# Performance work log

Measured on AMD Instinct MI355X. Metric: run time of the kernel, lower is better.

## Reference

```python
import jax, jax.numpy as jnp
import numpy as np

Q, B, D, NH, DH, DI, M = 1024, 4, 1024, 16, 64, 4096, 1024
K = Q + M  # klen
SCALE_W = 0.02
LN_EPS = 1e-5


def _layer_norm(x, g, b):
    mu = jnp.mean(x, axis=-1, keepdims=True)
    var = jnp.var(x, axis=-1, keepdims=True)
    return (x - mu) * jax.lax.rsqrt(var + LN_EPS) * g + b


def _rel_shift(x):
    # x: [qlen, klen, bsz, n_head] -> Transformer-XL relative shift
    q, k = x.shape[0], x.shape[1]
    zero_pad = jnp.zeros((q, 1) + x.shape[2:], x.dtype)
    x_padded = jnp.concatenate([zero_pad, x], axis=1)          # [q, k+1, b, n]
    x_padded = x_padded.reshape((k + 1, q) + x.shape[2:])      # [k+1, q, b, n]
    return x_padded[1:].reshape(x.shape)


def setup_inputs() -> dict:
    key = jax.random.key(0)
    ks = jax.random.split(key, 12)
    f32 = jnp.float32
    inp = {
        "w": jax.random.normal(ks[0], (Q, B, D), f32),
        "r": jax.random.normal(ks[1], (K, 1, D), f32),
        "mems": jax.random.normal(ks[2], (M, B, D), f32),
        "qkv_w": SCALE_W * jax.random.normal(ks[3], (D, 3 * NH * DH), f32),
        "r_net_w": SCALE_W * jax.random.normal(ks[4], (D, NH * DH), f32),
        "o_w": SCALE_W * jax.random.normal(ks[5], (NH * DH, D), f32),
        "r_w_bias": SCALE_W * jax.random.normal(ks[6], (NH, DH), f32),
        "r_r_bias": SCALE_W * jax.random.normal(ks[7], (NH, DH), f32),
        "ln1_g": jnp.ones((D,), f32),
        "ln1_b": jnp.zeros((D,), f32),
        "ff_w1": SCALE_W * jax.random.normal(ks[8], (D, DI), f32),
        "ff_b1": jnp.zeros((DI,), f32),
        "ff_w2": SCALE_W * jax.random.normal(ks[9], (DI, D), f32),
        "ff_b2": jnp.zeros((D,), f32),
        "ln2_g": jnp.ones((D,), f32),
        "ln2_b": jnp.zeros((D,), f32),
        # causal mask with memory: query i attends to keys j <= i + mem_len
        "attn_mask": jnp.arange(K)[None, :] > (jnp.arange(Q)[:, None] + M),
    }
    return inp


def reference(w, r, mems, qkv_w, r_net_w, o_w, r_w_bias, r_r_bias,
              ln1_g, ln1_b, ff_w1, ff_b1, ff_w2, ff_b2, ln2_g, ln2_b,
              attn_mask):
    qlen, bsz = w.shape[0], w.shape[1]
    # --- relative multi-head attention (post-lnorm, mems concat) ---
    cat = jnp.concatenate([mems, w], axis=0)                   # [klen, b, d]
    w_heads = cat @ qkv_w                                      # [klen, b, 3*nh*dh]
    r_head_k = (r @ r_net_w).reshape(-1, NH, DH)               # [rlen, nh, dh]
    q_h, k_h, v_h = jnp.split(w_heads, 3, axis=-1)
    klen = k_h.shape[0]
    q_h = q_h[-qlen:].reshape(qlen, bsz, NH, DH)
    k_h = k_h.reshape(klen, bsz, NH, DH)
    v_h = v_h.reshape(klen, bsz, NH, DH)

    rw_q = q_h + r_w_bias[None, None]                          # [q, b, nh, dh]
    AC = jnp.einsum('ibnd,jbnd->ijbn', rw_q, k_h)
    rr_q = q_h + r_r_bias[None, None]
    BD = jnp.einsum('ibnd,jnd->ijbn', rr_q, r_head_k)
    BD = _rel_shift(BD)

    scale = 1.0 / (DH ** 0.5)
    attn_score = (AC + BD) * scale                             # [q, k, b, nh]
    attn_score = jnp.where(attn_mask[:, :, None, None], -jnp.inf, attn_score)
    attn_prob = jax.nn.softmax(attn_score, axis=1)
    attn_vec = jnp.einsum('ijbn,jbnd->ibnd', attn_prob, v_h)
    attn_out = attn_vec.reshape(qlen, bsz, NH * DH) @ o_w      # [q, b, d]
    out = _layer_norm(w + attn_out, ln1_g, ln1_b)

    # --- position-wise FFN (post-lnorm) ---
    core = jax.nn.relu(out @ ff_w1 + ff_b1) @ ff_w2 + ff_b2
    out = _layer_norm(out + core, ln2_g, ln2_b)
    return out
```

## Files before the change

kernel.cpp:

```cpp
#include <hip/hip_runtime.h>
#include <math.h>


#define QLEN 1024
#define BSZ  4
#define DMODEL 1024
#define NHEAD 16
#define DHEAD 64
#define DINNER 4096
#define MEMLEN 1024
#define KLEN 2048

typedef __attribute__((ext_vector_type(8))) short short8;
typedef __attribute__((ext_vector_type(4))) short short4_t;
typedef __attribute__((ext_vector_type(4))) float f32x4;

__device__ __forceinline__ unsigned short f2bf(float x) {
  union { float f; unsigned u; } cv; cv.f = x;
  const unsigned u = cv.u;
  return (unsigned short)((u + 0x7FFFu + ((u >> 16) & 1u)) >> 16);
}
__device__ __forceinline__ float bf2f(unsigned short b) {
  union { unsigned u; float f; } cv; cv.u = ((unsigned)b) << 16;
  return cv.f;
}

__device__ __forceinline__ void gload16(const void* g, void* l) {
  __builtin_amdgcn_global_load_lds(
      (const __attribute__((address_space(1))) unsigned int*)g,
      (__attribute__((address_space(3))) unsigned int*)l, 16, 0, 0);
}

__device__ __forceinline__ int chidx(int row, int kc) {
  return row * 4 + (kc ^ ((row >> 1) & 3));
}

template<int MODE, int TN>
__global__ __launch_bounds__(256) void mgemm(
    const unsigned short* __restrict__ A, const unsigned short* __restrict__ Bt,
    float* __restrict__ C, unsigned short* __restrict__ Cb,
    const float* __restrict__ aux, const float* __restrict__ res,
    unsigned short* __restrict__ oK, unsigned short* __restrict__ oV,
    int Kdim, int N)
{
  __shared__ __align__(16) char smem[8192 + TN * 64];

  const int tid = threadIdx.x;
  const int lane = tid & 63, wv = tid >> 6;
  const int m0 = (int)blockIdx.y * 128, n0 = (int)blockIdx.x * TN;

  const unsigned short *gA0, *gA1, *gB0, *gB1 = nullptr;
  {
    int c = tid, m = c >> 2, kc = (c & 3) ^ ((m >> 1) & 3);
    gA0 = A + (size_t)(m0 + m) * Kdim + kc * 8;
    c = 256 + tid; m = c >> 2; kc = (c & 3) ^ ((m >> 1) & 3);
    gA1 = A + (size_t)(m0 + m) * Kdim + kc * 8;
    c = tid; int nn = c >> 2; kc = (c & 3) ^ ((nn >> 1) & 3);
    gB0 = Bt + (size_t)(n0 + nn) * Kdim + kc * 8;
    if constexpr (TN == 128) {
      c = 256 + tid; nn = c >> 2; kc = (c & 3) ^ ((nn >> 1) & 3);
      gB1 = Bt + (size_t)(n0 + nn) * Kdim + kc * 8;
    }
  }
  char* const lds0 = smem + (tid & 192) * 16;

  const int fr = lane & 15, kq = lane >> 4;
  constexpr int NJ = TN / 32;
  int aoff[4], boff[NJ];
#pragma unroll
  for (int t = 0; t < 4; ++t) {
    const int ra = (wv & 1) * 64 + t * 16 + fr;
    aoff[t] = chidx(ra, kq) * 16;
  }
#pragma unroll
  for (int t = 0; t < NJ; ++t) {
    const int rb = (wv >> 1) * (TN / 2) + t * 16 + fr;
    boff[t] = 8192 + chidx(rb, kq) * 16;
  }

  f32x4 acc[4][NJ] = {};

  for (int k0 = 0; k0 < Kdim; k0 += 32) {
    gload16(gA0, lds0);
    gload16(gA1, lds0 + 4096);
    gload16(gB0, lds0 + 8192);
    if constexpr (TN == 128) gload16(gB1, lds0 + 12288);
    gA0 += 32; gA1 += 32; gB0 += 32;
    if constexpr (TN == 128) gB1 += 32;
    __syncthreads();

    short8 af[4], bf[NJ];
#pragma unroll
    for (int t = 0; t < 4; ++t) af[t] = *(const short8*)(smem + aoff[t]);
#pragma unroll
    for (int t = 0; t < NJ; ++t) bf[t] = *(const short8*)(smem + boff[t]);
#pragma unroll
    for (int i = 0; i < 4; ++i)
#pragma unroll
      for (int j = 0; j < NJ; ++j)
        acc[i][j] = __builtin_amdgcn_mfma_f32_16x16x32_bf16(
            af[i], bf[j], acc[i][j], 0, 0, 0);
    __syncthreads();
  }

  const int rbase = m0 + (wv & 1) * 64 + (lane >> 4) * 4;
  const int cbase = n0 + (wv >> 1) * (TN / 2) + (lane & 15);
#pragma unroll
  for (int i = 0; i < 4; ++i) {
#pragma unroll
    for (int r = 0; r < 4; ++r) {
      const int grow = rbase + i * 16 + r;
#pragma unroll
      for (int j = 0; j < NJ; ++j) {
        const int gcol = cbase + j * 16;
        const float v = acc[i][j][r];
        if constexpr (MODE == 0) {
          const int kkg = grow >> 2, b2 = grow & 3;
          const int sec = gcol >> 10, hn = (gcol >> 6) & 15, d = gcol & 63;
          const unsigned short bv = f2bf(v);
          if (sec == 0) {
            if (kkg >= MEMLEN)
              Cb[((size_t)(b2 * NHEAD + hn) * QLEN + (kkg - MEMLEN)) * DHEAD + d] = bv;
          } else if (sec == 1) {
            oK[((size_t)(b2 * NHEAD + hn) * KLEN + kkg) * DHEAD + d] = bv;
          } else {
            oV[((size_t)(b2 * NHEAD + hn) * KLEN + kkg) * DHEAD + d] = bv;
          }
        } else if constexpr (MODE == 1) {
          const int hn = gcol >> 6, d = gcol & 63;
          Cb[((size_t)hn * KLEN + grow) * DHEAD + d] = f2bf(v);
        } else if constexpr (MODE == 2) {
          C[(size_t)grow * N + gcol] = v + res[(size_t)grow * N + gcol];
        } else if constexpr (MODE == 3) {
          Cb[(size_t)grow * N + gcol] = f2bf(fmaxf(v + aux[gcol], 0.f));
        } else {
          C[(size_t)grow * N + gcol] = v + aux[gcol] + res[(size_t)grow * N + gcol];
        }
      }
    }
  }
}

__global__ __launch_bounds__(256) void transpose_v(
    const unsigned short* __restrict__ Vh, unsigned short* __restrict__ Vt)
{
  __shared__ unsigned short t[64 * 80];
  const int j0 = (int)blockIdx.x * 64;
  const int bn = (int)blockIdx.y;
  const int tid = threadIdx.x;
#pragma unroll
  for (int it = 0; it < 2; ++it) {
    const int f = it * 256 + tid;
    const int j = f >> 3, d8 = (f & 7) * 8;
    const short8 v = *(const short8*)(Vh + ((size_t)bn * KLEN + j0 + j) * DHEAD + d8);
    *(short8*)(t + j * 80 + d8) = v;
  }
  __syncthreads();
  const int d = tid >> 2, jseg = (tid & 3) * 16;
  short8 o0, o1;
#pragma unroll
  for (int e = 0; e < 8; ++e) o0[e] = (short)t[(jseg + e) * 80 + d];
#pragma unroll
  for (int e = 0; e < 8; ++e) o1[e] = (short)t[(jseg + 8 + e) * 80 + d];
  unsigned short* op = Vt + ((size_t)bn * DHEAD + d) * KLEN + j0 + jseg;
  *(short8*)op = o0;
  *(short8*)(op + 8) = o1;
}

__global__ __launch_bounds__(256) void cast_all(
    const float* __restrict__ mems, const float* __restrict__ w,
    const float* __restrict__ r, unsigned short* __restrict__ Xcat,
    unsigned short* __restrict__ Rb16)
{
  const size_t i = ((size_t)blockIdx.x * 256 + threadIdx.x) * 8;
  const float* src;
  unsigned short* dst;
  if (i < 4194304)       { src = mems + i;          dst = Xcat + i; }
  else if (i < 8388608)  { src = w + (i - 4194304); dst = Xcat + i; }
  else                   { src = r + (i - 8388608); dst = Rb16 + (i - 8388608); }
  const float4 x = *(const float4*)src;
  const float4 y = *(const float4*)(src + 4);
  short8 v;
  v[0] = (short)f2bf(x.x); v[1] = (short)f2bf(x.y);
  v[2] = (short)f2bf(x.z); v[3] = (short)f2bf(x.w);
  v[4] = (short)f2bf(y.x); v[5] = (short)f2bf(y.y);
  v[6] = (short)f2bf(y.z); v[7] = (short)f2bf(y.w);
  *(short8*)dst = v;
}

__global__ __launch_bounds__(256) void transpose_all(
    const float* __restrict__ qkv_w, const float* __restrict__ r_net_w,
    const float* __restrict__ o_w, const float* __restrict__ ff_w1,
    const float* __restrict__ ff_w2,
    unsigned short* __restrict__ Wqkv, unsigned short* __restrict__ Wr,
    unsigned short* __restrict__ Wo, unsigned short* __restrict__ W1,
    unsigned short* __restrict__ W2)
{
  const int bid = (int)blockIdx.x;
  const float* in; unsigned short* out; int R, C, xt, loc;
  if (bid < 768)        { in = qkv_w;   out = Wqkv; R = 1024; C = 3072; xt = 48; loc = bid; }
  else if (bid < 1024)  { in = r_net_w; out = Wr;   R = 1024; C = 1024; xt = 16; loc = bid - 768; }
  else if (bid < 1280)  { in = o_w;     out = Wo;   R = 1024; C = 1024; xt = 16; loc = bid - 1024; }
  else if (bid < 2304)  { in = ff_w1;   out = W1;   R = 1024; C = 4096; xt = 64; loc = bid - 1280; }
  else                  { in = ff_w2;   out = W2;   R = 4096; C = 1024; xt = 16; loc = bid - 2304; }
  const int c0 = (loc % xt) * 64, r0 = (loc / xt) * 64;

  __shared__ float t[64][65];
  const int tid = threadIdx.x;
  const int rr = tid >> 4, cc = (tid & 15) * 4;
#pragma unroll
  for (int it = 0; it < 4; ++it) {
    const int rw = rr + it * 16;
    const float4 v = *(const float4*)(in + (size_t)(r0 + rw) * C + c0 + cc);
    t[rw][cc] = v.x; t[rw][cc + 1] = v.y; t[rw][cc + 2] = v.z; t[rw][cc + 3] = v.w;
  }
  __syncthreads();
  const int oc = tid >> 2, ob = (tid & 3) * 16;
#pragma unroll
  for (int j4 = 0; j4 < 4; ++j4) {
    short4_t o;
#pragma unroll
    for (int j = 0; j < 4; ++j) o[j] = (short)f2bf(t[ob + j4 * 4 + j][oc]);
    *(short4_t*)(out + (size_t)(c0 + oc) * R + r0 + ob + j4 * 4) = o;
  }
}

__global__ __launch_bounds__(256, 2) void attn_mfma(
    const unsigned short* __restrict__ Qh, const unsigned short* __restrict__ Kh,
    const unsigned short* __restrict__ Vt, const unsigned short* __restrict__ Rk,
    const float* __restrict__ rwb, const float* __restrict__ rrb,
    float* __restrict__ Opart0, float* __restrict__ Opart1,
    float* __restrict__ den0, float* __restrict__ den1)
{
  __shared__ __align__(16) char smem[65536];

  const int tid = threadIdx.x;
  const int lane = tid & 63, wv = tid >> 6;
  const int quad = lane >> 4, l15 = lane & 15;

  const int bid0 = (int)blockIdx.y * 32 + (int)blockIdx.x;
  const int slot = bid0 >> 3;
  const int bn = (bid0 & 7) * 8 + (slot >> 5);
  const int inner = slot & 31;
  const int it = inner >> 1, sp = inner & 1;
  const int i0 = it * 64;
  const int n = bn & 15;

  const int nch = 17 + it;
  const int h = (nch + 1) >> 1;
  const int lo = sp ? h : 0, hi = sp ? nch : h;

  const unsigned short* __restrict__ Qb = Qh + (size_t)bn * QLEN * DHEAD;
  const unsigned short* __restrict__ Kb = Kh + (size_t)bn * KLEN * DHEAD;
  const unsigned short* __restrict__ Vb = Vt + (size_t)bn * DHEAD * KLEN;
  const unsigned short* __restrict__ Rb = Rk + (size_t)n * KLEN * DHEAD;

  short8 qk[2], qr[2];
  {
    const int qrow = i0 + wv * 16 + l15;
    const unsigned short* qp = Qb + (size_t)qrow * DHEAD + quad * 8;
    const float* wp = rwb + n * DHEAD + quad * 8;
    const float* rp = rrb + n * DHEAD + quad * 8;
#pragma unroll
    for (int ks = 0; ks < 2; ++ks) {
      const short8 q8 = *(const short8*)(qp + ks * 32);
#pragma unroll
      for (int e = 0; e < 8; ++e) {
        const float qv = bf2f((unsigned short)q8[e]);
        qk[ks][e] = (short)f2bf(qv + wp[ks * 32 + e]);
        qr[ks][e] = (short)f2bf(qv + rp[ks * 32 + e]);
      }
    }
  }

  int srcl[4];
  bool condE[4];
#pragma unroll
  for (int r = 0; r < 4; ++r) {
    const int E = l15 - quad * 4 - r + 15;
    srcl[r] = (lane & 48) | (E & 15);
    condE[r] = (E >= 16);
  }

  f32x4 O[4] = {};
  float rden[4] = {0.f, 0.f, 0.f, 0.f};
  const int wvoff = (tid & 192) * 16;

  {
    const int j0 = lo * 64;
    const int g64 = lo - it + 15;
    const int rb3 = (g64 % 3) * 64;
#pragma unroll
    for (int t2 = 0; t2 < 2; ++t2) {
      const int s = t2 * 256 + tid;
      const int row = s >> 3, kc = (s & 7) ^ (row & 7);
      gload16(Kb + (((size_t)(j0 + row)) << 6) + kc * 8,
              smem + t2 * 4096 + wvoff);
    }
#pragma unroll
    for (int t2 = 0; t2 < 2; ++t2) {
      const int s = t2 * 256 + tid;
      const int row = s >> 3, kc = (s & 7) ^ (row & 7);
      gload16(Vb + (((size_t)row) << 11) + j0 + kc * 8,
              smem + 16384 + t2 * 4096 + wvoff);
    }
    const int gw = j0 - i0 + 960;
#pragma unroll
    for (int t2 = 0; t2 < 4; ++t2) {
      const int rr = t2 * 32 + (tid >> 3);
      const int gr = gw + rr;
      const int kc = (tid & 7) ^ (rr & 7);
      int pb = rb3 + t2 * 32; if (pb >= 192) pb -= 192;
      gload16(Rb + (((size_t)gr) << 6) + kc * 8,
              smem + 32768 + pb * 128 + wvoff);
    }
  }

  int cur = 0;
  for (int ch = lo; ch < hi; ++ch) {
    const int j0 = ch * 64;
    const int g64 = ch - it + 15;
    const int rb3 = (g64 % 3) * 64;
    const int gw = j0 - i0 + 960;

    asm volatile("s_waitcnt lgkmcnt(0)" ::: "memory");
    __builtin_amdgcn_s_barrier();

    if (ch + 1 < hi) {
      const int nb = cur ^ 1;
      const int j0n = j0 + 64;
#pragma unroll
      for (int t2 = 0; t2 < 2; ++t2) {
        const int s = t2 * 256 + tid;
        const int row = s >> 3, kc = (s & 7) ^ (row & 7);
        gload16(Kb + (((size_t)(j0n + row)) << 6) + kc * 8,
                smem + nb * 8192 + t2 * 4096 + wvoff);
      }
#pragma unroll
      for (int t2 = 0; t2 < 2; ++t2) {
        const int s = t2 * 256 + tid;
        const int row = s >> 3, kc = (s & 7) ^ (row & 7);
        gload16(Vb + (((size_t)row) << 11) + j0n + kc * 8,
                smem + 16384 + nb * 8192 + t2 * 4096 + wvoff);
      }
#pragma unroll
      for (int t2 = 0; t2 < 2; ++t2) {
        const int rr = t2 * 32 + (tid >> 3);
        const int gr = gw + 128 + rr;
        const int kc = (tid & 7) ^ (rr & 7);
        int pb = rb3 + 128 + t2 * 32; if (pb >= 192) pb -= 192;
        gload16(Rb + (((size_t)gr) << 6) + kc * 8,
                smem + 32768 + pb * 128 + wvoff);
      }
      asm volatile("s_waitcnt vmcnt(6)" ::: "memory");
    } else {
      asm volatile("s_waitcnt vmcnt(0)" ::: "memory");
    }
    __builtin_amdgcn_s_barrier();

    const char* const kbase = smem + cur * 8192;
    const char* const vbase = smem + 16384 + cur * 8192;

    f32x4 sk[4];
#pragma unroll
    for (int jt = 0; jt < 4; ++jt) {
      f32x4 a = {0.f, 0.f, 0.f, 0.f};
#pragma unroll
      for (int ks = 0; ks < 2; ++ks) {
        const int frr = jt * 16 + l15;
        const int c = (ks * 4 + quad) ^ (l15 & 7);
        const short8 kf = *(const short8*)(kbase + (frr * 8 + c) * 16);
        a = __builtin_amdgcn_mfma_f32_16x16x32_bf16(qk[ks], kf, a, 0, 0, 0);
      }
      sk[jt] = a;
    }
    f32x4 uu[5];
#pragma unroll
    for (int s = 0; s < 5; ++s) {
      f32x4 a = {0.f, 0.f, 0.f, 0.f};
      int frr = rb3 + (3 - wv + s) * 16 + l15;
      if (frr >= 192) frr -= 192;
#pragma unroll
      for (int ks = 0; ks < 2; ++ks) {
        const int c = (ks * 4 + quad) ^ (l15 & 7);
        const short8 rf = *(const short8*)(smem + 32768 + (frr * 8 + c) * 16);
        a = __builtin_amdgcn_mfma_f32_16x16x32_bf16(qr[ks], rf, a, 0, 0, 0);
      }
      uu[s] = a;
    }

    float rot[5][4];
#pragma unroll
    for (int s = 0; s < 5; ++s)
#pragma unroll
      for (int r = 0; r < 4; ++r)
        rot[s][r] = __shfl(uu[s][r], srcl[r], 64);

    unsigned short* const Ps = (unsigned short*)(smem + 57344);
#pragma unroll
    for (int jt = 0; jt < 4; ++jt) {
      const int jl = jt * 16 + l15;
#pragma unroll
      for (int r = 0; r < 4; ++r) {
        const int il = wv * 16 + quad * 4 + r;
        const int dj = (j0 + jl) - (i0 + il);
        const float uv = condE[r] ? rot[jt + 1][r] : rot[jt][r];
        const float sv = (sk[jt][r] + uv) * 0.125f;
        const float p = (dj <= 1024) ? __expf(sv) : 0.f;
        rden[r] += p;
        Ps[(il * 8 + ((jl >> 3) ^ (il & 7))) * 8 + (jl & 7)] = f2bf(p);
      }
    }

#pragma unroll
    for (int ks = 0; ks < 2; ++ks) {
      const int frp = wv * 16 + l15;
      const int cp = (ks * 4 + quad) ^ (l15 & 7);
      const short8 pf = *(const short8*)(smem + 57344 + (frp * 8 + cp) * 16);
#pragma unroll
      for (int dt = 0; dt < 4; ++dt) {
        const int vr = dt * 16 + l15;
        const short8 vf = *(const short8*)(vbase + (vr * 8 + cp) * 16);
        O[dt] = __builtin_amdgcn_mfma_f32_16x16x32_bf16(pf, vf, O[dt], 0, 0, 0);
      }
    }
    cur ^= 1;
  }

#pragma unroll
  for (int m = 1; m < 16; m <<= 1)
#pragma unroll
    for (int r = 0; r < 4; ++r)
      rden[r] += __shfl_xor(rden[r], m, 64);

  float* const Op = sp ? Opart1 : Opart0;
  float* const dp = sp ? den1 : den0;
  const size_t ob = (size_t)(bn * 16 + it) * 64;
#pragma unroll
  for (int r = 0; r < 4; ++r) {
    const int il = wv * 16 + quad * 4 + r;
#pragma unroll
    for (int dt = 0; dt < 4; ++dt)
      Op[(ob + il) * 64 + dt * 16 + l15] = O[dt][r];
    if (l15 == 0) dp[ob + il] = rden[r];
  }
}

__global__ __launch_bounds__(256) void attn_combine(
    const float* __restrict__ O0, const float* __restrict__ O1,
    const float* __restrict__ d0, const float* __restrict__ d1,
    unsigned short* __restrict__ AVb)
{
  const int blk = (int)blockIdx.x;
  const int bn = blk >> 4, it = blk & 15;
  const int b = bn >> 4, n = bn & 15;
  const int tid = threadIdx.x;
  const int il = tid >> 2, ds = (tid & 3) * 16;
  const size_t base = ((size_t)blk * 64 + il) * 64 + ds;
  const float inv = 1.f / (d0[blk * 64 + il] + d1[blk * 64 + il]);
  short8 o0, o1;
#pragma unroll
  for (int g = 0; g < 2; ++g) {
    const float4 a = *(const float4*)(O0 + base + g * 8);
    const float4 bb = *(const float4*)(O1 + base + g * 8);
    const float4 a2 = *(const float4*)(O0 + base + g * 8 + 4);
    const float4 b2 = *(const float4*)(O1 + base + g * 8 + 4);
    short8& o = g ? o1 : o0;
    o[0] = (short)f2bf((a.x + bb.x) * inv);  o[1] = (short)f2bf((a.y + bb.y) * inv);
    o[2] = (short)f2bf((a.z + bb.z) * inv);  o[3] = (short)f2bf((a.w + bb.w) * inv);
    o[4] = (short)f2bf((a2.x + b2.x) * inv); o[5] = (short)f2bf((a2.y + b2.y) * inv);
    o[6] = (short)f2bf((a2.z + b2.z) * inv); o[7] = (short)f2bf((a2.w + b2.w) * inv);
  }
  unsigned short* op =
      AVb + ((size_t)(it * 64 + il) * BSZ + b) * DMODEL + n * DHEAD + ds;
  *(short8*)op = o0;
  *(short8*)(op + 8) = o1;
}

__global__ __launch_bounds__(256) void ln_kernel(
    float* __restrict__ X, const float* __restrict__ gw,
    const float* __restrict__ bw, unsigned short* __restrict__ bfo)
{
  const int row = blockIdx.x, tid = threadIdx.x;
  float* rp = X + (size_t)row * DMODEL;
  const float4 x = *(const float4*)(rp + tid * 4);
  float s = x.x + x.y + x.z + x.w;
  float q = x.x * x.x + x.y * x.y + x.z * x.z + x.w * x.w;
#pragma unroll
  for (int m = 1; m < 64; m <<= 1) {
    s += __shfl_xor(s, m, 64);
    q += __shfl_xor(q, m, 64);
  }
  __shared__ float ss[4], sq[4];
  if ((tid & 63) == 0) { ss[tid >> 6] = s; sq[tid >> 6] = q; }
  __syncthreads();
  s = ss[0] + ss[1] + ss[2] + ss[3];
  q = sq[0] + sq[1] + sq[2] + sq[3];
  const float mu = s * (1.f / DMODEL);
  const float var = q * (1.f / DMODEL) - mu * mu;
  const float rstd = rsqrtf(var + 1e-5f);
  const float4 g4 = *(const float4*)(gw + tid * 4);
  const float4 b4 = *(const float4*)(bw + tid * 4);
  float4 y;
  y.x = (x.x - mu) * rstd * g4.x + b4.x;
  y.y = (x.y - mu) * rstd * g4.y + b4.y;
  y.z = (x.z - mu) * rstd * g4.z + b4.z;
  y.w = (x.w - mu) * rstd * g4.w + b4.w;
  *(float4*)(rp + tid * 4) = y;
  if (bfo) {
    short4_t o;
    o[0] = (short)f2bf(y.x); o[1] = (short)f2bf(y.y);
    o[2] = (short)f2bf(y.z); o[3] = (short)f2bf(y.w);
    *(short4_t*)(bfo + (size_t)row * DMODEL + tid * 4) = o;
  }
}

extern "C" void kernel_launch(void* const* d_in, const int* in_sizes, int n_in,
                              void* d_out, int out_size, void* d_ws,
                              size_t ws_size, hipStream_t stream)
{
  const float* w       = (const float*)d_in[0];
  const float* r       = (const float*)d_in[1];
  const float* mems    = (const float*)d_in[2];
  const float* qkv_w   = (const float*)d_in[3];
  const float* r_net_w = (const float*)d_in[4];
  const float* o_w     = (const float*)d_in[5];
  const float* r_w_bias= (const float*)d_in[6];
  const float* r_r_bias= (const float*)d_in[7];
  const float* ln1_g   = (const float*)d_in[8];
  const float* ln1_b   = (const float*)d_in[9];
  const float* ff_w1   = (const float*)d_in[10];
  const float* ff_b1   = (const float*)d_in[11];
  const float* ff_w2   = (const float*)d_in[12];
  const float* ff_b2   = (const float*)d_in[13];
  const float* ln2_g   = (const float*)d_in[14];
  const float* ln2_b   = (const float*)d_in[15];
  float* out = (float*)d_out;

  float* X1 = (float*)d_ws;
  unsigned short* Qh   = (unsigned short*)(X1 + 4194304);
  unsigned short* Kh   = Qh + 4194304;
  unsigned short* Vt   = Kh + 8388608;
  unsigned short* Rk   = Vt + 8388608;
  unsigned short* Xcat = Rk + 2097152 + 8192;
  unsigned short* Wqkv = Xcat + 8388608;
  unsigned short* Wr   = Wqkv + 3145728;
  unsigned short* Wo   = Wr + 1048576;
  unsigned short* W1   = Wo + 1048576;
  unsigned short* W2   = W1 + 4194304;
  float* den0 = (float*)(W2 + 4194304);
  float* den1 = den0 + 65536;
  unsigned short* AVb  = (unsigned short*)(den1 + 65536);
  unsigned short* Vh     = (unsigned short*)X1;
  unsigned short* Rb16   = AVb;
  float* Opart0          = (float*)X1;
  float* Opart1          = (float*)Xcat;
  unsigned short* X1b    = Qh;
  unsigned short* H      = Kh;

  const dim3 blk(256);

  cast_all<<<dim3(5120), blk, 0, stream>>>(mems, w, r, Xcat, Rb16);
  transpose_all<<<dim3(3328), blk, 0, stream>>>(
      qkv_w, r_net_w, o_w, ff_w1, ff_w2, Wqkv, Wr, Wo, W1, W2);

  mgemm<0, 128><<<dim3(24, 64), blk, 0, stream>>>(
      Xcat, Wqkv, nullptr, Qh, nullptr, nullptr, Kh, Vh, DMODEL, 3 * DMODEL);
  transpose_v<<<dim3(32, 64), blk, 0, stream>>>(Vh, Vt);
  mgemm<1, 64><<<dim3(16, 16), blk, 0, stream>>>(
      Rb16, Wr, nullptr, Rk, nullptr, nullptr, nullptr, nullptr, DMODEL, DMODEL);
  attn_mfma<<<dim3(32, 64), blk, 0, stream>>>(
      Qh, Kh, Vt, Rk, r_w_bias, r_r_bias, Opart0, Opart1, den0, den1);
  attn_combine<<<dim3(1024), blk, 0, stream>>>(Opart0, Opart1, den0, den1, AVb);
  mgemm<2, 64><<<dim3(16, 32), blk, 0, stream>>>(
      AVb, Wo, X1, nullptr, nullptr, w, nullptr, nullptr, DMODEL, DMODEL);
  ln_kernel<<<dim3(4096), blk, 0, stream>>>(X1, ln1_g, ln1_b, X1b);
  mgemm<3, 128><<<dim3(32, 32), blk, 0, stream>>>(
      X1b, W1, nullptr, H, ff_b1, nullptr, nullptr, nullptr, DMODEL, DINNER);
  mgemm<4, 64><<<dim3(16, 32), blk, 0, stream>>>(
      H, W2, out, nullptr, ff_b2, X1, nullptr, nullptr, DINNER, DMODEL);
  ln_kernel<<<dim3(4096), blk, 0, stream>>>(out, ln2_g, ln2_b, nullptr);

  (void)in_sizes; (void)n_in; (void)out_size; (void)ws_size;
}
```

Before: 559.0 us.

## Double-buffer GEMM LDS loads, swizzle workgroup order, and cheapen attention exp/mask

The GEMM main loop now double-buffers its LDS tiles, issuing the next k-slice's global-to-LDS loads before computing on the current one and using explicit vmcnt waits and raw barriers instead of two full __syncthreads per step. Workgroup indices are remapped in groups of eight to change which tiles run concurrently, which may help L2 reuse. In attention, exp is computed as exp2f with the scale folded into one constant, and the causal mask check is skipped except on the diagonal chunk. The changes double GEMM LDS use, which may lower occupancy, and the hand-written waitcnt counts must match the number of loads in flight.

New measurement: 527.5 us. 5.6% less time.

```diff
diff --git a/kernel.cpp b/kernel.cpp
--- a/kernel.cpp
+++ b/kernel.cpp
@@ -43,11 +43,17 @@
     unsigned short* __restrict__ oK, unsigned short* __restrict__ oV,
     int Kdim, int N)
 {
-  __shared__ __align__(16) char smem[8192 + TN * 64];
+  constexpr int BUF = 8192 + TN * 64;
+  __shared__ __align__(16) char smem[2 * BUF];
 
   const int tid = threadIdx.x;
   const int lane = tid & 63, wv = tid >> 6;
-  const int m0 = (int)blockIdx.y * 128, n0 = (int)blockIdx.x * TN;
+
+  const int gx = (int)gridDim.x;
+  const int nwg = gx * (int)gridDim.y;
+  const int flat = (int)blockIdx.y * gx + (int)blockIdx.x;
+  const int swz = (flat & 7) * (nwg >> 3) + (flat >> 3);
+  const int m0 = (swz / gx) * 128, n0 = (swz % gx) * TN;
 
   const unsigned short *gA0, *gA1, *gB0, *gB1 = nullptr;
   {
@@ -62,7 +68,7 @@
       gB1 = Bt + (size_t)(n0 + nn) * Kdim + kc * 8;
     }
   }
-  char* const lds0 = smem + (tid & 192) * 16;
+  const int wvoff = (tid & 192) * 16;
 
   const int fr = lane & 15, kq = lane >> 4;
   constexpr int NJ = TN / 32;
@@ -80,27 +86,51 @@
 
   f32x4 acc[4][NJ] = {};
 
-  for (int k0 = 0; k0 < Kdim; k0 += 32) {
-    gload16(gA0, lds0);
-    gload16(gA1, lds0 + 4096);
-    gload16(gB0, lds0 + 8192);
-    if constexpr (TN == 128) gload16(gB1, lds0 + 12288);
+  {
+    char* const b0 = smem + wvoff;
+    gload16(gA0, b0);
+    gload16(gA1, b0 + 4096);
+    gload16(gB0, b0 + 8192);
+    if constexpr (TN == 128) gload16(gB1, b0 + 12288);
     gA0 += 32; gA1 += 32; gB0 += 32;
     if constexpr (TN == 128) gB1 += 32;
-    __syncthreads();
-
-    short8 af[4], bf[NJ];
-#pragma unroll
-    for (int t = 0; t < 4; ++t) af[t] = *(const short8*)(smem + aoff[t]);
-#pragma unroll
-    for (int t = 0; t < NJ; ++t) bf[t] = *(const short8*)(smem + boff[t]);
+  }
+
+  int cur = 0;
+  for (int k0 = 0; k0 < Kdim; k0 += 32) {
+    if (k0 + 32 < Kdim) {
+      char* const nb = smem + (cur ^ 1) * BUF + wvoff;
+      gload16(gA0, nb);
+      gload16(gA1, nb + 4096);
+      gload16(gB0, nb + 8192);
+      if constexpr (TN == 128) gload16(gB1, nb + 12288);
+      gA0 += 32; gA1 += 32; gB0 += 32;
+      if constexpr (TN == 128) gB1 += 32;
+      if constexpr (TN == 128)
+        asm volatile("s_waitcnt vmcnt(4)" ::: "memory");
+      else
+        asm volatile("s_waitcnt vmcnt(3)" ::: "memory");
+    } else {
+      asm volatile("s_waitcnt vmcnt(0)" ::: "memory");
+    }
+    __builtin_amdgcn_s_barrier();
+
+    const char* const cb = smem + cur * BUF;
+    short8 af[4], bfr[NJ];
+#pragma unroll
+    for (int t = 0; t < 4; ++t) af[t] = *(const short8*)(cb + aoff[t]);
+#pragma unroll
+    for (int t = 0; t < NJ; ++t) bfr[t] = *(const short8*)(cb + boff[t]);
 #pragma unroll
     for (int i = 0; i < 4; ++i)
 #pragma unroll
       for (int j = 0; j < NJ; ++j)
         acc[i][j] = __builtin_amdgcn_mfma_f32_16x16x32_bf16(
-            af[i], bf[j], acc[i][j], 0, 0, 0);
-    __syncthreads();
+            af[i], bfr[j], acc[i][j], 0, 0, 0);
+
+    asm volatile("s_waitcnt lgkmcnt(0)" ::: "memory");
+    __builtin_amdgcn_s_barrier();
+    cur ^= 1;
   }
 
   const int rbase = m0 + (wv & 1) * 64 + (lane >> 4) * 4;
@@ -397,16 +427,20 @@
         rot[s][r] = __shfl(uu[s][r], srcl[r], 64);
 
     unsigned short* const Ps = (unsigned short*)(smem + 57344);
+    constexpr float CE = 0.18033688f;
+    const bool needmask = (ch - it) == 16;
 #pragma unroll
     for (int jt = 0; jt < 4; ++jt) {
       const int jl = jt * 16 + l15;
 #pragma unroll
       for (int r = 0; r < 4; ++r) {
         const int il = wv * 16 + quad * 4 + r;
-        const int dj = (j0 + jl) - (i0 + il);
         const float uv = condE[r] ? rot[jt + 1][r] : rot[jt][r];
-        const float sv = (sk[jt][r] + uv) * 0.125f;
-        const float p = (dj <= 1024) ? __expf(sv) : 0.f;
+        float p = exp2f((sk[jt][r] + uv) * CE);
+        if (needmask) {
+          const int dj = (j0 + jl) - (i0 + il);
+          if (dj > 1024) p = 0.f;
+        }
         rden[r] += p;
         Ps[(il * 8 + ((jl >> 3) ^ (il & 7))) * 8 + (jl & 7)] = f2bf(p);
       }
```
